# Performance work log

Measured on AMD Instinct MI355X. Metric: run time of the kernel, lower is better.

The kernel has to match this reference:

```python
import jax, jax.numpy as jnp
import numpy as np

H, C_K, C_Q = 4, 512, 512


def setup_inputs() -> dict:
    key = jax.random.key(0)
    ks = jax.random.split(key, 6)
    s = 1.0 / np.sqrt(512.0)
    return {
        "x_k": jax.random.normal(ks[0], (4096, 512), jnp.float32),
        "x_q": jax.random.normal(ks[1], (4096, 512), jnp.float32),
        "k_w": jax.random.normal(ks[2], (H * C_K, 512), jnp.float32) * s,
        "q_w": jax.random.normal(ks[3], (H * C_Q, 512), jnp.float32) * s,
        "attn_w": jax.random.normal(ks[4], (H, C_K, C_Q), jnp.float32) * s,
        "proj_w": jax.random.normal(ks[5], (C_K, C_Q), jnp.float32) * s,
    }


def reference(x_k, x_q, k_w, q_w, attn_w, proj_w):
    # Project keys/queries and split into heads: [H, N, c]
    xk = (x_k @ k_w.T).reshape(-1, H, C_K).transpose(1, 0, 2)
    xq = (x_q @ q_w.T).reshape(-1, H, C_Q).transpose(1, 0, 2)
    # Bilinear scores: alphas[h, n, m] = xk[h,n,:] @ attn_w[h] @ xq[h,m,:]
    alphas = jnp.einsum("hnk,hkq,hmq->hnm", xk, attn_w, xq)
    # key-side update
    alpha_ks = jax.nn.softmax(alphas, axis=2)                 # [H, Nk, Nq]
    alpha_k_agg = jnp.mean(jnp.einsum("hnm,hmq->hnq", alpha_ks, xq), axis=0)
    x_k_update = alpha_k_agg @ proj_w.T                       # [Nk, C_K]
    # query-side update (bidirectional)
    alpha_qs = jax.nn.softmax(alphas.transpose(0, 2, 1), axis=2)  # [H, Nq, Nk]
    alpha_q_agg = jnp.mean(jnp.einsum("hmn,hnk->hmk", alpha_qs, xk), axis=0)
    x_q_update = alpha_q_agg @ proj_w                         # [Nq, C_Q]
    return x_k + x_k_update, x_q + x_q_update
```

## Files before the change

### kernel.cpp

```cpp
#include <hip/hip_runtime.h>
#include <stdint.h>

#define DEVI __device__ __forceinline__

typedef unsigned short u16;
typedef unsigned int u32;
typedef __attribute__((ext_vector_type(4))) unsigned short u16x4;
typedef __attribute__((ext_vector_type(8))) unsigned short u16x8;
typedef __attribute__((ext_vector_type(4))) float f32x4;
typedef __attribute__((ext_vector_type(8))) _Float16 f16x8;

static constexpr int NT = 4096;
static constexpr int D  = 512;
static constexpr int NH = 4;
static constexpr int KS = 4;

DEVI u16 f2h(float f) {
  _Float16 h = (_Float16)f;
  union { _Float16 h; u16 u; } v; v.h = h;
  return v.u;
}
DEVI float h2f(u16 u) {
  union { u16 u; _Float16 h; } v; v.u = u;
  return (float)v.h;
}

DEVI u32 enc_ord(float f) {
  u32 u = __float_as_uint(f);
  return (u & 0x80000000u) ? ~u : (u | 0x80000000u);
}
DEVI float dec_ord(u32 k) {
  u32 u = (k & 0x80000000u) ? (k ^ 0x80000000u) : ~k;
  return __uint_as_float(u);
}

DEVI void gld_lds16(const u16* g, u16* l) {
  __builtin_amdgcn_global_load_lds((const __attribute__((address_space(1))) void*)g,
                                   (__attribute__((address_space(3))) void*)l, 16, 0, 0);
}

enum { OUT_F32 = 0, OUT_F16 = 2, OUT_RES = 3, OUT_SMAX = 4, OUT_F16T = 5 };

template<int OUT>
__global__ __launch_bounds__(256)
void gemm_bt(const u16* __restrict__ A, int lda, size_t zsA,
             const u16* __restrict__ B, int ldb, size_t zsB,
             void* __restrict__ Cp, int ldc, size_t zsC,
             const float* __restrict__ res, int K,
             u32* __restrict__ rmg, u32* __restrict__ cmg,
             u16* __restrict__ STp, int ldct)
{
  constexpr bool DOT = (OUT == OUT_SMAX || OUT == OUT_F16T);
  __shared__ u16 As[128 * 32];
  __shared__ u16 Bs[128 * 32];
  __shared__ u32 rmaxs[128], cmaxs[128];
  __shared__ u16 Tt[DOT ? 128 * 72 : 8];
  A += blockIdx.z * zsA;
  B += blockIdx.z * zsB;
  const int tid = threadIdx.x;
  const int lane = tid & 63, w = tid >> 6;
  const int wr = w >> 1, wc = w & 1;
  const int m0 = blockIdx.y * 128, n0 = blockIdx.x * 128;

  if (OUT == OUT_SMAX && tid < 128) { rmaxs[tid] = 0u; cmaxs[tid] = 0u; }

  f32x4 acc[4][4] = {};

  for (int k0 = 0; k0 < K; k0 += 32) {
    __syncthreads();
#pragma unroll
    for (int p = 0; p < 2; ++p) {
      int id = p * 256 + tid;
      int row = id >> 2, q = id & 3;
      gld_lds16(A + (size_t)(m0 + row) * lda + k0 + q * 8, As + id * 8);
      gld_lds16(B + (size_t)(n0 + row) * ldb + k0 + q * 8, Bs + id * 8);
    }
    __syncthreads();
    f16x8 af[4], bfv[4];
#pragma unroll
    for (int i = 0; i < 4; ++i)
      af[i] = *(const f16x8*)(As + (wr * 64 + i * 16 + (lane & 15)) * 32 + (lane >> 4) * 8);
#pragma unroll
    for (int i = 0; i < 4; ++i)
      bfv[i] = *(const f16x8*)(Bs + (wc * 64 + i * 16 + (lane & 15)) * 32 + (lane >> 4) * 8);
#pragma unroll
    for (int i = 0; i < 4; ++i)
#pragma unroll
      for (int j = 0; j < 4; ++j)
        acc[i][j] = __builtin_amdgcn_mfma_f32_16x16x32_f16(af[i], bfv[j], acc[i][j], 0, 0, 0);
  }

#pragma unroll
  for (int i = 0; i < 4; ++i) {
    int rl0 = wr * 64 + i * 16 + (lane >> 4) * 4;
#pragma unroll
    for (int j = 0; j < 4; ++j) {
      int c = n0 + wc * 64 + j * 16 + (lane & 15);
#pragma unroll
      for (int e = 0; e < 4; ++e) {
        size_t idx = blockIdx.z * zsC + (size_t)(m0 + rl0 + e) * ldc + c;
        float v = acc[i][j][e];
        if (OUT == OUT_F32)  ((float*)Cp)[idx] = v;
        if (OUT == OUT_F16)  ((u16*)Cp)[idx] = f2h(v);
        if (OUT == OUT_RES)  ((float*)Cp)[idx] = res[idx] + v;
        if (OUT == OUT_SMAX || OUT == OUT_F16T) ((u16*)Cp)[idx] = f2h(v);
      }
    }
  }

  if (OUT == OUT_SMAX) {
#pragma unroll
    for (int i = 0; i < 4; ++i) {
      int rl0 = wr * 64 + i * 16 + (lane >> 4) * 4;
#pragma unroll
      for (int e = 0; e < 4; ++e) {
        float m = fmaxf(fmaxf(acc[i][0][e], acc[i][1][e]), fmaxf(acc[i][2][e], acc[i][3][e]));
        atomicMax(&rmaxs[rl0 + e], enc_ord(m));
      }
    }
#pragma unroll
    for (int j = 0; j < 4; ++j) {
      float m = -3e38f;
#pragma unroll
      for (int i = 0; i < 4; ++i)
#pragma unroll
        for (int e = 0; e < 4; ++e) m = fmaxf(m, acc[i][j][e]);
      atomicMax(&cmaxs[wc * 64 + j * 16 + (lane & 15)], enc_ord(m));
    }
    __syncthreads();
    if (tid < 128) {
      atomicMax(rmg + m0 + tid, rmaxs[tid]);
      atomicMax(cmg + n0 + tid, cmaxs[tid]);
    }
  }

  if (DOT) {
#pragma unroll
    for (int half = 0; half < 2; ++half) {
      __syncthreads();
      if (wr == half) {
#pragma unroll
        for (int i = 0; i < 4; ++i) {
          int rl = i * 16 + (lane >> 4) * 4;
#pragma unroll
          for (int j = 0; j < 4; ++j) {
            int cl = wc * 64 + j * 16 + (lane & 15);
            u16x4 v;
            v[0] = f2h(acc[i][j][0]); v[1] = f2h(acc[i][j][1]);
            v[2] = f2h(acc[i][j][2]); v[3] = f2h(acc[i][j][3]);
            *(u16x4*)&Tt[cl * 72 + rl] = v;
          }
        }
      }
      __syncthreads();
#pragma unroll
      for (int q = 0; q < 4; ++q) {
        int id2 = q * 256 + tid;
        int c = id2 >> 3, mm = (id2 & 7) * 8;
        u16x8 v = *(const u16x8*)&Tt[c * 72 + mm];
        *(u16x8*)(STp + (size_t)(n0 + c) * ldct + m0 + half * 64 + mm) = v;
      }
    }
  }
}

__global__ __launch_bounds__(256)
void pv(const u16* __restrict__ Sarg, const u32* __restrict__ mx_u,
        const u16* __restrict__ B,
        u16* __restrict__ part, float* __restrict__ lpart, int Ksl)
{
  __shared__ u16 As[64 * 40];
  __shared__ u16 Bs[128 * 32];
  __shared__ float ps[4][64];
  const int tid = threadIdx.x;
  const int lane = tid & 63, w = tid >> 6;
  const int wr = w >> 1, wc = w & 1;
  const int m0 = blockIdx.y * 64, n0 = blockIdx.x * 128;
  const int kb = blockIdx.z * Ksl;

  const int rA = tid >> 2, kc = (tid & 3) * 8;
  const float mxA = dec_ord(mx_u[m0 + rA]);
  const u16* S0 = Sarg + (size_t)(m0 + rA) * NT + kb + kc;

  f32x4 acc[2][4] = {};
  float sacc = 0.f;

  f16x8 sv0 = *(const f16x8*)S0;

  for (int k0 = 0; k0 < Ksl; k0 += 32) {
    __syncthreads();
#pragma unroll
    for (int p = 0; p < 2; ++p) {
      int id = p * 256 + tid;
      int row = id >> 2, q = id & 3;
      gld_lds16(B + (size_t)(n0 + row) * NT + kb + k0 + q * 8, Bs + id * 8);
    }
    f16x8 nx0;
    if (k0 + 32 < Ksl) nx0 = *(const f16x8*)(S0 + k0 + 32);
    {
      u16x8 pk;
      float rs = 0.f;
#pragma unroll
      for (int j = 0; j < 8; ++j) {
        float e = __expf((float)sv0[j] - mxA);
        rs += e; pk[j] = f2h(e);
      }
      *(u16x8*)(As + rA * 40 + kc) = pk;
      sacc += rs;
    }
    __syncthreads();
    f16x8 af[2], bfv[4];
#pragma unroll
    for (int i = 0; i < 2; ++i)
      af[i] = *(const f16x8*)(As + (wr * 32 + i * 16 + (lane & 15)) * 40 + (lane >> 4) * 8);
#pragma unroll
    for (int j = 0; j < 4; ++j)
      bfv[j] = *(const f16x8*)(Bs + (wc * 64 + j * 16 + (lane & 15)) * 32 + (lane >> 4) * 8);
#pragma unroll
    for (int i = 0; i < 2; ++i)
#pragma unroll
      for (int j = 0; j < 4; ++j)
        acc[i][j] = __builtin_amdgcn_mfma_f32_16x16x32_f16(af[i], bfv[j], acc[i][j], 0, 0, 0);
    sv0 = nx0;
  }

  u16* out = part + (size_t)blockIdx.z * NT * D;
#pragma unroll
  for (int i = 0; i < 2; ++i) {
    int r0 = m0 + wr * 32 + i * 16 + (lane >> 4) * 4;
#pragma unroll
    for (int j = 0; j < 4; ++j) {
      int c = n0 + wc * 64 + j * 16 + (lane & 15);
#pragma unroll
      for (int e = 0; e < 4; ++e)
        out[(size_t)(r0 + e) * D + c] = f2h(acc[i][j][e]);
    }
  }

  __syncthreads();
  ps[tid & 3][tid >> 2] = sacc;
  __syncthreads();
  if (blockIdx.x == 0 && tid < 64) {
    lpart[(size_t)blockIdx.z * NT + m0 + tid] =
        ps[0][tid] + ps[1][tid] + ps[2][tid] + ps[3][tid];
  }
}

__global__ __launch_bounds__(256)
void reduce2(const u16* __restrict__ pk, const float* __restrict__ lk,
             const u16* __restrict__ pq, const float* __restrict__ lq,
             float* __restrict__ out0, float* __restrict__ out1)
{
  const size_t i = ((size_t)blockIdx.x * 256 + threadIdx.x) * 4;
  const int m = (int)(i >> 9);
  const size_t zs = (size_t)NT * D;
  float Lk = 0.f, Lq = 0.f;
#pragma unroll
  for (int z = 0; z < KS; ++z) { Lk += lk[(size_t)z * NT + m]; Lq += lq[(size_t)z * NT + m]; }
  float s0 = 0.f, s1 = 0.f, s2 = 0.f, s3 = 0.f;
#pragma unroll
  for (int z = 0; z < KS; ++z) {
    u16x4 v = *(const u16x4*)(pk + z * zs + i);
    s0 += h2f(v[0]); s1 += h2f(v[1]); s2 += h2f(v[2]); s3 += h2f(v[3]);
  }
  f32x4 o = *(const f32x4*)(out0 + i);
  float ck = 0.25f / Lk;
  o[0] += s0 * ck; o[1] += s1 * ck; o[2] += s2 * ck; o[3] += s3 * ck;
  *(f32x4*)(out0 + i) = o;
  s0 = s1 = s2 = s3 = 0.f;
#pragma unroll
  for (int z = 0; z < KS; ++z) {
    u16x4 v = *(const u16x4*)(pq + z * zs + i);
    s0 += h2f(v[0]); s1 += h2f(v[1]); s2 += h2f(v[2]); s3 += h2f(v[3]);
  }
  f32x4 p = *(const f32x4*)(out1 + i);
  float cq = 0.25f / Lq;
  p[0] += s0 * cq; p[1] += s1 * cq; p[2] += s2 * cq; p[3] += s3 * cq;
  *(f32x4*)(out1 + i) = p;
}

__global__ __launch_bounds__(256)
void cast_f32_f16(const float* __restrict__ in, u16* __restrict__ out, int n)
{
  int i = (blockIdx.x * 256 + threadIdx.x) * 8;
  if (i >= n) return;
  f32x4 a = *(const f32x4*)(in + i), b = *(const f32x4*)(in + i + 4);
  u16x8 s;
  s[0] = f2h(a[0]); s[1] = f2h(a[1]); s[2] = f2h(a[2]); s[3] = f2h(a[3]);
  s[4] = f2h(b[0]); s[5] = f2h(b[1]); s[6] = f2h(b[2]); s[7] = f2h(b[3]);
  *(u16x8*)(out + i) = s;
}

__global__ __launch_bounds__(256)
void transpose_cast_f32(const float* __restrict__ in, int ldi,
                        u16* __restrict__ out, int ldo)
{
  __shared__ u16 t[64][72];
  int r0 = blockIdx.x * 64, c0 = blockIdx.y * 64;
  int t8 = threadIdx.x & 7, rr = threadIdx.x >> 3;
#pragma unroll
  for (int p = 0; p < 2; ++p) {
    int r = rr + p * 32;
    const float* src = in + (size_t)(r0 + r) * ldi + c0 + t8 * 8;
    f32x4 a = *(const f32x4*)src, b = *(const f32x4*)(src + 4);
    u16x8 s;
    s[0] = f2h(a[0]); s[1] = f2h(a[1]); s[2] = f2h(a[2]); s[3] = f2h(a[3]);
    s[4] = f2h(b[0]); s[5] = f2h(b[1]); s[6] = f2h(b[2]); s[7] = f2h(b[3]);
    *(u16x8*)&t[r][t8 * 8] = s;
  }
  __syncthreads();
#pragma unroll
  for (int p = 0; p < 2; ++p) {
    int c = rr + p * 32;
    u16x8 s;
#pragma unroll
    for (int j = 0; j < 8; ++j) s[j] = t[t8 * 8 + j][c];
    *(u16x8*)(out + (size_t)(c0 + c) * ldo + r0 + t8 * 8) = s;
  }
}

extern "C" void kernel_launch(void* const* d_in, const int* in_sizes, int n_in,
                              void* d_out, int out_size, void* d_ws, size_t ws_size,
                              hipStream_t stream)
{
  const float* x_k    = (const float*)d_in[0];
  const float* x_q    = (const float*)d_in[1];
  const float* k_w    = (const float*)d_in[2];
  const float* q_w    = (const float*)d_in[3];
  const float* attn_w = (const float*)d_in[4];
  const float* proj_w = (const float*)d_in[5];
  float* out0 = (float*)d_out;
  float* out1 = out0 + (size_t)NT * D;

  char* wptr = (char*)d_ws;
  auto alloc = [&](size_t bytes) { char* p = wptr; wptr += (bytes + 255) & ~(size_t)255; return p; };
  u16*   pb     = (u16*)  alloc((size_t)D * D * 2);
  u16*   pbT    = (u16*)  alloc((size_t)D * D * 2);
  u16*   XKall  = (u16*)  alloc((size_t)NT * NH * D * 2);
  u16*   XKTall = (u16*)  alloc((size_t)NT * NH * D * 2);
  u16*   XQTall = (u16*)  alloc((size_t)NT * NH * D * 2);
  u16*   Kpall  = (u16*)  alloc((size_t)NH * NT * D * 2);
  u16*   partK  = (u16*)  alloc((size_t)KS * NT * D * 2);
  u16*   partQ  = (u16*)  alloc((size_t)KS * NT * D * 2);
  float* lk     = (float*)alloc((size_t)KS * NT * 4);
  float* lq     = (float*)alloc((size_t)KS * NT * 4);
  u32*   rowm_u = (u32*)  alloc((size_t)NT * 4);
  u32*   colm_u = (u32*)  alloc((size_t)NT * 4);
  u16*   ST     = (u16*)  alloc((size_t)NT * NT * 2);
  char*  Sreg   = alloc((size_t)NT * NT * 2);
  u16*   S      = (u16*)Sreg;
  char* sp = Sreg;
  auto salloc = [&](size_t bytes) { char* p = sp; sp += (bytes + 255) & ~(size_t)255; return p; };
  u16* xkb   = (u16*)salloc((size_t)NT * D * 2);
  u16* xqb   = (u16*)salloc((size_t)NT * D * 2);
  u16* kwb   = (u16*)salloc((size_t)NH * D * D * 2);
  u16* qwb   = (u16*)salloc((size_t)NH * D * D * 2);
  u16* Abf   = (u16*)salloc((size_t)NH * D * D * 2);
  u16* XQall = (u16*)salloc((size_t)NT * NH * D * 2);

  cast_f32_f16<<<NT * D / 2048, 256, 0, stream>>>(x_k, xkb, NT * D);
  cast_f32_f16<<<NT * D / 2048, 256, 0, stream>>>(x_q, xqb, NT * D);
  cast_f32_f16<<<NH * D * D / 2048, 256, 0, stream>>>(k_w, kwb, NH * D * D);
  cast_f32_f16<<<NH * D * D / 2048, 256, 0, stream>>>(q_w, qwb, NH * D * D);
  cast_f32_f16<<<NH * D * D / 2048, 256, 0, stream>>>(attn_w, Abf, NH * D * D);
  cast_f32_f16<<<D * D / 2048, 256, 0, stream>>>(proj_w, pb, D * D);
  transpose_cast_f32<<<dim3(D / 64, D / 64), 256, 0, stream>>>(proj_w, D, pbT, D);

  gemm_bt<OUT_F16T><<<dim3(NH * D / 128, NT / 128), 256, 0, stream>>>(
      xkb, D, 0, kwb, D, 0, XKall, NH * D, 0, nullptr, D, nullptr, nullptr, XKTall, NT);
  gemm_bt<OUT_F16T><<<dim3(NH * D / 128, NT / 128), 256, 0, stream>>>(
      xqb, D, 0, qwb, D, 0, XQall, NH * D, 0, nullptr, D, nullptr, nullptr, XQTall, NT);
  gemm_bt<OUT_F16><<<dim3(D / 128, NT / 128, NH), 256, 0, stream>>>(
      XQall, NH * D, (size_t)D, Abf, D, (size_t)D * D, Kpall, D, (size_t)NT * D, nullptr, D,
      nullptr, nullptr, nullptr, 0);

  hipMemsetAsync(d_out, 0, (size_t)2 * NT * D * 4, stream);

  for (int h = 0; h < NH; ++h) {
    const u16* XKh  = XKall + (size_t)h * D;
    const u16* XKTh = XKTall + (size_t)h * D * NT;
    const u16* XQTh = XQTall + (size_t)h * D * NT;
    const u16* Kph  = Kpall + (size_t)h * NT * D;

    hipMemsetAsync(rowm_u, 0, (size_t)NT * 4 * 2, stream);

    gemm_bt<OUT_SMAX><<<dim3(NT / 128, NT / 128), 256, 0, stream>>>(
        XKh, NH * D, 0, Kph, D, 0, S, NT, 0, nullptr, D, rowm_u, colm_u, ST, NT);

    pv<<<dim3(D / 128, NT / 64, KS), 256, 0, stream>>>(
        S, rowm_u, XQTh, partK, lk, NT / KS);
    pv<<<dim3(D / 128, NT / 64, KS), 256, 0, stream>>>(
        ST, colm_u, XKTh, partQ, lq, NT / KS);

    reduce2<<<NT * D / 1024, 256, 0, stream>>>(partK, lk, partQ, lq, out0, out1);
  }

  u16* kf16 = partK;
  u16* qf16 = partK + (size_t)NT * D;
  cast_f32_f16<<<NT * D / 2048, 256, 0, stream>>>(out0, kf16, NT * D);
  cast_f32_f16<<<NT * D / 2048, 256, 0, stream>>>(out1, qf16, NT * D);
  gemm_bt<OUT_RES><<<dim3(D / 128, NT / 128), 256, 0, stream>>>(
      kf16, D, 0, pb, D, 0, out0, D, 0, x_k, D, nullptr, nullptr, nullptr, 0);
  gemm_bt<OUT_RES><<<dim3(D / 128, NT / 128), 256, 0, stream>>>(
      qf16, D, 0, pbT, D, 0, out1, D, 0, x_q, D, nullptr, nullptr, nullptr, 0);
}
```

Before: 635.4 us.

## Merge key/query PV launches, stage DOT epilogue through LDS, fuse final cast

The two per-head pv launches become one pv2 launch whose z dimension selects either the key-side or the query-side problem, doubling the grid and removing a launch per head. The DOT-variant GEMM epilogue now writes the row-major S tile through LDS with 16-byte vector stores instead of scattered 2-byte stores. The final f32-to-f16 casts are folded into the last reduce2 call via an emit flag, removing two kernel launches and a re-read of the outputs. This adds extra syncthreads and LDS traffic in the GEMM epilogue, and reuses the S region for the f16 outputs after it is last read.

```diff
diff --git a/kernel.cpp b/kernel.cpp
--- a/kernel.cpp
+++ b/kernel.cpp
@@ -90,20 +90,21 @@
         acc[i][j] = __builtin_amdgcn_mfma_f32_16x16x32_f16(af[i], bfv[j], acc[i][j], 0, 0, 0);
   }
 
-#pragma unroll
-  for (int i = 0; i < 4; ++i) {
-    int rl0 = wr * 64 + i * 16 + (lane >> 4) * 4;
-#pragma unroll
-    for (int j = 0; j < 4; ++j) {
-      int c = n0 + wc * 64 + j * 16 + (lane & 15);
-#pragma unroll
-      for (int e = 0; e < 4; ++e) {
-        size_t idx = blockIdx.z * zsC + (size_t)(m0 + rl0 + e) * ldc + c;
-        float v = acc[i][j][e];
-        if (OUT == OUT_F32)  ((float*)Cp)[idx] = v;
-        if (OUT == OUT_F16)  ((u16*)Cp)[idx] = f2h(v);
-        if (OUT == OUT_RES)  ((float*)Cp)[idx] = res[idx] + v;
-        if (OUT == OUT_SMAX || OUT == OUT_F16T) ((u16*)Cp)[idx] = f2h(v);
+  if (!DOT) {
+#pragma unroll
+    for (int i = 0; i < 4; ++i) {
+      int rl0 = wr * 64 + i * 16 + (lane >> 4) * 4;
+#pragma unroll
+      for (int j = 0; j < 4; ++j) {
+        int c = n0 + wc * 64 + j * 16 + (lane & 15);
+#pragma unroll
+        for (int e = 0; e < 4; ++e) {
+          size_t idx = blockIdx.z * zsC + (size_t)(m0 + rl0 + e) * ldc + c;
+          float v = acc[i][j][e];
+          if (OUT == OUT_F32) ((float*)Cp)[idx] = v;
+          if (OUT == OUT_F16) ((u16*)Cp)[idx] = f2h(v);
+          if (OUT == OUT_RES) ((float*)Cp)[idx] = res[idx] + v;
+        }
       }
     }
   }
@@ -135,6 +136,31 @@
   }
 
   if (DOT) {
+#pragma unroll
+    for (int chalf = 0; chalf < 2; ++chalf) {
+      __syncthreads();
+      if (wc == chalf) {
+#pragma unroll
+        for (int i = 0; i < 4; ++i) {
+          int rl0 = wr * 64 + i * 16 + (lane >> 4) * 4;
+#pragma unroll
+          for (int j = 0; j < 4; ++j) {
+            int c63 = j * 16 + (lane & 15);
+#pragma unroll
+            for (int e = 0; e < 4; ++e)
+              Tt[(rl0 + e) * 72 + c63] = f2h(acc[i][j][e]);
+          }
+        }
+      }
+      __syncthreads();
+#pragma unroll
+      for (int q = 0; q < 4; ++q) {
+        int id2 = q * 256 + tid;
+        int r = id2 >> 3, c8 = (id2 & 7) * 8;
+        u16x8 v = *(const u16x8*)&Tt[r * 72 + c8];
+        *(u16x8*)((u16*)Cp + blockIdx.z * zsC + (size_t)(m0 + r) * ldc + n0 + chalf * 64 + c8) = v;
+      }
+    }
 #pragma unroll
     for (int half = 0; half < 2; ++half) {
       __syncthreads();
@@ -165,18 +191,29 @@
 }
 
 __global__ __launch_bounds__(256)
-void pv(const u16* __restrict__ Sarg, const u32* __restrict__ mx_u,
-        const u16* __restrict__ B,
-        u16* __restrict__ part, float* __restrict__ lpart, int Ksl)
+void pv2(const u16* __restrict__ S, const u16* __restrict__ ST,
+         const u32* __restrict__ rowm_u, const u32* __restrict__ colm_u,
+         const u16* __restrict__ BQ, const u16* __restrict__ BK,
+         u16* __restrict__ partK, u16* __restrict__ partQ,
+         float* __restrict__ lk, float* __restrict__ lq, int Ksl)
 {
   __shared__ u16 As[64 * 40];
   __shared__ u16 Bs[128 * 32];
   __shared__ float ps[4][64];
+  const int z8 = blockIdx.z;
+  const bool d2 = z8 >= KS;
+  const int z = d2 ? z8 - KS : z8;
+  const u16* Sarg = d2 ? ST : S;
+  const u32* mx_u = d2 ? colm_u : rowm_u;
+  const u16* B    = d2 ? BK : BQ;
+  u16* part       = d2 ? partQ : partK;
+  float* lpart    = d2 ? lq : lk;
+
   const int tid = threadIdx.x;
   const int lane = tid & 63, w = tid >> 6;
   const int wr = w >> 1, wc = w & 1;
   const int m0 = blockIdx.y * 64, n0 = blockIdx.x * 128;
-  const int kb = blockIdx.z * Ksl;
+  const int kb = z * Ksl;
 
   const int rA = tid >> 2, kc = (tid & 3) * 8;
   const float mxA = dec_ord(mx_u[m0 + rA]);
@@ -224,7 +261,7 @@
     sv0 = nx0;
   }
 
-  u16* out = part + (size_t)blockIdx.z * NT * D;
+  u16* out = part + (size_t)z * NT * D;
 #pragma unroll
   for (int i = 0; i < 2; ++i) {
     int r0 = m0 + wr * 32 + i * 16 + (lane >> 4) * 4;
@@ -241,7 +278,7 @@
   ps[tid & 3][tid >> 2] = sacc;
   __syncthreads();
   if (blockIdx.x == 0 && tid < 64) {
-    lpart[(size_t)blockIdx.z * NT + m0 + tid] =
+    lpart[(size_t)z * NT + m0 + tid] =
         ps[0][tid] + ps[1][tid] + ps[2][tid] + ps[3][tid];
   }
 }
@@ -249,7 +286,8 @@
 __global__ __launch_bounds__(256)
 void reduce2(const u16* __restrict__ pk, const float* __restrict__ lk,
              const u16* __restrict__ pq, const float* __restrict__ lq,
-             float* __restrict__ out0, float* __restrict__ out1)
+             float* __restrict__ out0, float* __restrict__ out1,
+             u16* __restrict__ o0h, u16* __restrict__ o1h, int emit)
 {
   const size_t i = ((size_t)blockIdx.x * 256 + threadIdx.x) * 4;
   const int m = (int)(i >> 9);
@@ -267,6 +305,10 @@
   float ck = 0.25f / Lk;
   o[0] += s0 * ck; o[1] += s1 * ck; o[2] += s2 * ck; o[3] += s3 * ck;
   *(f32x4*)(out0 + i) = o;
+  if (emit) {
+    u16x4 hh; hh[0] = f2h(o[0]); hh[1] = f2h(o[1]); hh[2] = f2h(o[2]); hh[3] = f2h(o[3]);
+    *(u16x4*)(o0h + i) = hh;
+  }
   s0 = s1 = s2 = s3 = 0.f;
 #pragma unroll
   for (int z = 0; z < KS; ++z) {
@@ -277,6 +319,10 @@
   float cq = 0.25f / Lq;
   p[0] += s0 * cq; p[1] += s1 * cq; p[2] += s2 * cq; p[3] += s3 * cq;
   *(f32x4*)(out1 + i) = p;
+  if (emit) {
+    u16x4 hh; hh[0] = f2h(p[0]); hh[1] = f2h(p[1]); hh[2] = f2h(p[2]); hh[3] = f2h(p[3]);
+    *(u16x4*)(o1h + i) = hh;
+  }
 }
 
 __global__ __launch_bounds__(256)
@@ -357,6 +403,8 @@
   u16* qwb   = (u16*)salloc((size_t)NH * D * D * 2);
   u16* Abf   = (u16*)salloc((size_t)NH * D * D * 2);
   u16* XQall = (u16*)salloc((size_t)NT * NH * D * 2);
+  u16* kf16 = (u16*)Sreg;
+  u16* qf16 = (u16*)Sreg + (size_t)NT * D;
 
   cast_f32_f16<<<NT * D / 2048, 256, 0, stream>>>(x_k, xkb, NT * D);
   cast_f32_f16<<<NT * D / 2048, 256, 0, stream>>>(x_q, xqb, NT * D);
@@ -387,18 +435,13 @@
     gemm_bt<OUT_SMAX><<<dim3(NT / 128, NT / 128), 256, 0, stream>>>(
         XKh, NH * D, 0, Kph, D, 0, S, NT, 0, nullptr, D, rowm_u, colm_u, ST, NT);
 
-    pv<<<dim3(D / 128, NT / 64, KS), 256, 0, stream>>>(
-        S, rowm_u, XQTh, partK, lk, NT / KS);
-    pv<<<dim3(D / 128, NT / 64, KS), 256, 0, stream>>>(
-        ST, colm_u, XKTh, partQ, lq, NT / KS);
-
-    reduce2<<<NT * D / 1024, 256, 0, stream>>>(partK, lk, partQ, lq, out0, out1);
-  }
-
-  u16* kf16 = partK;
-  u16* qf16 = partK + (size_t)NT * D;
-  cast_f32_f16<<<NT * D / 2048, 256, 0, stream>>>(out0, kf16, NT * D);
-  cast_f32_f16<<<NT * D / 2048, 256, 0, stream>>>(out1, qf16, NT * D);
+    pv2<<<dim3(D / 128, NT / 64, 2 * KS), 256, 0, stream>>>(
+        S, ST, rowm_u, colm_u, XQTh, XKTh, partK, partQ, lk, lq, NT / KS);
+
+    reduce2<<<NT * D / 1024, 256, 0, stream>>>(
+        partK, lk, partQ, lq, out0, out1, kf16, qf16, h == NH - 1 ? 1 : 0);
+  }
+
   gemm_bt<OUT_RES><<<dim3(D / 128, NT / 128), 256, 0, stream>>>(
       kf16, D, 0, pb, D, 0, out0, D, 0, x_k, D, nullptr, nullptr, nullptr, 0);
   gemm_bt<OUT_RES><<<dim3(D / 128, NT / 128), 256, 0, stream>>>(
```

Measured after the change: 632.6 us. About the same (-0.4%).

## Batch projection GEMMs via z-dim, accumulate aggregates in fp16, coalesce DOT stores

Applied to the files above, without the earlier changes.

The K and Q projection GEMMs are merged into one launch using blockIdx.z, and so are the two final residual GEMMs. The per-head aggregate accumulators become fp16 buffers, which removes the fp32 output memset, the two cast kernels and the fp32 read-modify-write traffic in reduce2. The direct row-major output of the DOT GEMM variants is restaged through LDS so it is written as 16-byte coalesced stores. Accumulating across heads in fp16 loses some precision, and the extra LDS staging pass adds barriers.

```diff
diff --git a/kernel.cpp b/kernel.cpp
--- a/kernel.cpp
+++ b/kernel.cpp
@@ -46,9 +46,9 @@
 void gemm_bt(const u16* __restrict__ A, int lda, size_t zsA,
              const u16* __restrict__ B, int ldb, size_t zsB,
              void* __restrict__ Cp, int ldc, size_t zsC,
-             const float* __restrict__ res, int K,
+             const float* __restrict__ res, const float* __restrict__ res2, int K,
              u32* __restrict__ rmg, u32* __restrict__ cmg,
-             u16* __restrict__ STp, int ldct)
+             u16* __restrict__ STp, int ldct, size_t zsT)
 {
   constexpr bool DOT = (OUT == OUT_SMAX || OUT == OUT_F16T);
   __shared__ u16 As[128 * 32];
@@ -57,6 +57,7 @@
   __shared__ u16 Tt[DOT ? 128 * 72 : 8];
   A += blockIdx.z * zsA;
   B += blockIdx.z * zsB;
+  const float* resz = (OUT == OUT_RES && blockIdx.z) ? res2 : res;
   const int tid = threadIdx.x;
   const int lane = tid & 63, w = tid >> 6;
   const int wr = w >> 1, wc = w & 1;
@@ -90,20 +91,21 @@
         acc[i][j] = __builtin_amdgcn_mfma_f32_16x16x32_f16(af[i], bfv[j], acc[i][j], 0, 0, 0);
   }
 
-#pragma unroll
-  for (int i = 0; i < 4; ++i) {
-    int rl0 = wr * 64 + i * 16 + (lane >> 4) * 4;
-#pragma unroll
-    for (int j = 0; j < 4; ++j) {
-      int c = n0 + wc * 64 + j * 16 + (lane & 15);
-#pragma unroll
-      for (int e = 0; e < 4; ++e) {
-        size_t idx = blockIdx.z * zsC + (size_t)(m0 + rl0 + e) * ldc + c;
-        float v = acc[i][j][e];
-        if (OUT == OUT_F32)  ((float*)Cp)[idx] = v;
-        if (OUT == OUT_F16)  ((u16*)Cp)[idx] = f2h(v);
-        if (OUT == OUT_RES)  ((float*)Cp)[idx] = res[idx] + v;
-        if (OUT == OUT_SMAX || OUT == OUT_F16T) ((u16*)Cp)[idx] = f2h(v);
+  if (!DOT) {
+#pragma unroll
+    for (int i = 0; i < 4; ++i) {
+      int rl0 = wr * 64 + i * 16 + (lane >> 4) * 4;
+#pragma unroll
+      for (int j = 0; j < 4; ++j) {
+        int c = n0 + wc * 64 + j * 16 + (lane & 15);
+#pragma unroll
+        for (int e = 0; e < 4; ++e) {
+          size_t idx = blockIdx.z * zsC + (size_t)(m0 + rl0 + e) * ldc + c;
+          float v = acc[i][j][e];
+          if (OUT == OUT_F32) ((float*)Cp)[idx] = v;
+          if (OUT == OUT_F16) ((u16*)Cp)[idx] = f2h(v);
+          if (OUT == OUT_RES) ((float*)Cp)[idx] = resz[(size_t)(m0 + rl0 + e) * ldc + c] + v;
+        }
       }
     }
   }
@@ -135,6 +137,31 @@
   }
 
   if (DOT) {
+#pragma unroll
+    for (int chalf = 0; chalf < 2; ++chalf) {
+      __syncthreads();
+      if (wc == chalf) {
+#pragma unroll
+        for (int i = 0; i < 4; ++i) {
+          int rl0 = wr * 64 + i * 16 + (lane >> 4) * 4;
+#pragma unroll
+          for (int j = 0; j < 4; ++j) {
+            int c63 = j * 16 + (lane & 15);
+#pragma unroll
+            for (int e = 0; e < 4; ++e)
+              Tt[(rl0 + e) * 72 + c63] = f2h(acc[i][j][e]);
+          }
+        }
+      }
+      __syncthreads();
+#pragma unroll
+      for (int q = 0; q < 4; ++q) {
+        int id2 = q * 256 + tid;
+        int r = id2 >> 3, c8 = (id2 & 7) * 8;
+        u16x8 v = *(const u16x8*)&Tt[r * 72 + c8];
+        *(u16x8*)((u16*)Cp + blockIdx.z * zsC + (size_t)(m0 + r) * ldc + n0 + chalf * 64 + c8) = v;
+      }
+    }
 #pragma unroll
     for (int half = 0; half < 2; ++half) {
       __syncthreads();
@@ -158,7 +185,7 @@
         int id2 = q * 256 + tid;
         int c = id2 >> 3, mm = (id2 & 7) * 8;
         u16x8 v = *(const u16x8*)&Tt[c * 72 + mm];
-        *(u16x8*)(STp + (size_t)(n0 + c) * ldct + m0 + half * 64 + mm) = v;
+        *(u16x8*)(STp + blockIdx.z * zsT + (size_t)(n0 + c) * ldct + m0 + half * 64 + mm) = v;
       }
     }
   }
@@ -249,7 +276,7 @@
 __global__ __launch_bounds__(256)
 void reduce2(const u16* __restrict__ pk, const float* __restrict__ lk,
              const u16* __restrict__ pq, const float* __restrict__ lq,
-             float* __restrict__ out0, float* __restrict__ out1)
+             u16* __restrict__ a0h, u16* __restrict__ a1h)
 {
   const size_t i = ((size_t)blockIdx.x * 256 + threadIdx.x) * 4;
   const int m = (int)(i >> 9);
@@ -263,20 +290,24 @@
     u16x4 v = *(const u16x4*)(pk + z * zs + i);
     s0 += h2f(v[0]); s1 += h2f(v[1]); s2 += h2f(v[2]); s3 += h2f(v[3]);
   }
-  f32x4 o = *(const f32x4*)(out0 + i);
   float ck = 0.25f / Lk;
-  o[0] += s0 * ck; o[1] += s1 * ck; o[2] += s2 * ck; o[3] += s3 * ck;
-  *(f32x4*)(out0 + i) = o;
+  u16x4 a = *(const u16x4*)(a0h + i);
+  u16x4 na;
+  na[0] = f2h(h2f(a[0]) + s0 * ck); na[1] = f2h(h2f(a[1]) + s1 * ck);
+  na[2] = f2h(h2f(a[2]) + s2 * ck); na[3] = f2h(h2f(a[3]) + s3 * ck);
+  *(u16x4*)(a0h + i) = na;
   s0 = s1 = s2 = s3 = 0.f;
 #pragma unroll
   for (int z = 0; z < KS; ++z) {
     u16x4 v = *(const u16x4*)(pq + z * zs + i);
     s0 += h2f(v[0]); s1 += h2f(v[1]); s2 += h2f(v[2]); s3 += h2f(v[3]);
   }
-  f32x4 p = *(const f32x4*)(out1 + i);
   float cq = 0.25f / Lq;
-  p[0] += s0 * cq; p[1] += s1 * cq; p[2] += s2 * cq; p[3] += s3 * cq;
-  *(f32x4*)(out1 + i) = p;
+  u16x4 b = *(const u16x4*)(a1h + i);
+  u16x4 nb;
+  nb[0] = f2h(h2f(b[0]) + s0 * cq); nb[1] = f2h(h2f(b[1]) + s1 * cq);
+  nb[2] = f2h(h2f(b[2]) + s2 * cq); nb[3] = f2h(h2f(b[3]) + s3 * cq);
+  *(u16x4*)(a1h + i) = nb;
 }
 
 __global__ __launch_bounds__(256)
@@ -342,6 +373,8 @@
   u16*   Kpall  = (u16*)  alloc((size_t)NH * NT * D * 2);
   u16*   partK  = (u16*)  alloc((size_t)KS * NT * D * 2);
   u16*   partQ  = (u16*)  alloc((size_t)KS * NT * D * 2);
+  u16*   agg0h  = (u16*)  alloc((size_t)NT * D * 2);
+  u16*   agg1h  = (u16*)  alloc((size_t)NT * D * 2);
   float* lk     = (float*)alloc((size_t)KS * NT * 4);
   float* lq     = (float*)alloc((size_t)KS * NT * 4);
   u32*   rowm_u = (u32*)  alloc((size_t)NT * 4);
@@ -366,15 +399,15 @@
   cast_f32_f16<<<D * D / 2048, 256, 0, stream>>>(proj_w, pb, D * D);
   transpose_cast_f32<<<dim3(D / 64, D / 64), 256, 0, stream>>>(proj_w, D, pbT, D);
 
-  gemm_bt<OUT_F16T><<<dim3(NH * D / 128, NT / 128), 256, 0, stream>>>(
-      xkb, D, 0, kwb, D, 0, XKall, NH * D, 0, nullptr, D, nullptr, nullptr, XKTall, NT);
-  gemm_bt<OUT_F16T><<<dim3(NH * D / 128, NT / 128), 256, 0, stream>>>(
-      xqb, D, 0, qwb, D, 0, XQall, NH * D, 0, nullptr, D, nullptr, nullptr, XQTall, NT);
+  gemm_bt<OUT_F16T><<<dim3(NH * D / 128, NT / 128, 2), 256, 0, stream>>>(
+      xkb, D, (size_t)(xqb - xkb), kwb, D, (size_t)(qwb - kwb),
+      XKall, NH * D, (size_t)(XQall - XKall), nullptr, nullptr, D,
+      nullptr, nullptr, XKTall, NT, (size_t)(XQTall - XKTall));
   gemm_bt<OUT_F16><<<dim3(D / 128, NT / 128, NH), 256, 0, stream>>>(
-      XQall, NH * D, (size_t)D, Abf, D, (size_t)D * D, Kpall, D, (size_t)NT * D, nullptr, D,
-      nullptr, nullptr, nullptr, 0);
-
-  hipMemsetAsync(d_out, 0, (size_t)2 * NT * D * 4, stream);
+      XQall, NH * D, (size_t)D, Abf, D, (size_t)D * D, Kpall, D, (size_t)NT * D,
+      nullptr, nullptr, D, nullptr, nullptr, nullptr, 0, 0);
+
+  hipMemsetAsync(agg0h, 0, (size_t)2 * NT * D * 2, stream);
 
   for (int h = 0; h < NH; ++h) {
     const u16* XKh  = XKall + (size_t)h * D;
@@ -385,22 +418,18 @@
     hipMemsetAsync(rowm_u, 0, (size_t)NT * 4 * 2, stream);
 
     gemm_bt<OUT_SMAX><<<dim3(NT / 128, NT / 128), 256, 0, stream>>>(
-        XKh, NH * D, 0, Kph, D, 0, S, NT, 0, nullptr, D, rowm_u, colm_u, ST, NT);
+        XKh, NH * D, 0, Kph, D, 0, S, NT, 0, nullptr, nullptr, D,
+        rowm_u, colm_u, ST, NT, 0);
 
     pv<<<dim3(D / 128, NT / 64, KS), 256, 0, stream>>>(
         S, rowm_u, XQTh, partK, lk, NT / KS);
     pv<<<dim3(D / 128, NT / 64, KS), 256, 0, stream>>>(
         ST, colm_u, XKTh, partQ, lq, NT / KS);
 
-    reduce2<<<NT * D / 1024, 256, 0, stream>>>(partK, lk, partQ, lq, out0, out1);
-  }
-
-  u16* kf16 = partK;
-  u16* qf16 = partK + (size_t)NT * D;
-  cast_f32_f16<<<NT * D / 2048, 256, 0, stream>>>(out0, kf16, NT * D);
-  cast_f32_f16<<<NT * D / 2048, 256, 0, stream>>>(out1, qf16, NT * D);
-  gemm_bt<OUT_RES><<<dim3(D / 128, NT / 128), 256, 0, stream>>>(
-      kf16, D, 0, pb, D, 0, out0, D, 0, x_k, D, nullptr, nullptr, nullptr, 0);
-  gemm_bt<OUT_RES><<<dim3(D / 128, NT / 128), 256, 0, stream>>>(
-      qf16, D, 0, pbT, D, 0, out1, D, 0, x_q, D, nullptr, nullptr, nullptr, 0);
-}
+    reduce2<<<NT * D / 1024, 256, 0, stream>>>(partK, lk, partQ, lq, agg0h, agg1h);
+  }
+
+  gemm_bt<OUT_RES><<<dim3(D / 128, NT / 128, 2), 256, 0, stream>>>(
+      agg0h, D, (size_t)(agg1h - agg0h), pb, D, (size_t)(pbT - pb),
+      out0, D, (size_t)NT * D, x_k, x_q, D, nullptr, nullptr, nullptr, 0, 0);
+}
```

After: 606.3 us. 1.05x faster.
